# Kernel tuning notes

Hardware: AMD Instinct MI355X
Metric: run time of the kernel (lower is better)

The kernel has to match this reference:

```python
import jax, jax.numpy as jnp
import numpy as np

N_TILE = 50000
N_POI = 50000
E = 200000
IN_F = 128
HID = 256
OUT = 256
HEADS = 8
NEG_SLOPE = 0.2


def gatv2(hs, hd, src, dst, Wsrc, bsrc, Wdst, bdst, attn, n_dst):
    """DGL GATv2Conv: per-edge LeakyReLU(fs_u + fd_v) attention, edge-softmax over
    incoming edges of each dst node, attention-weighted sum of source features.
    Returns (n_dst, H*D) (already flattened, matching .flatten(1))."""
    H, D = attn.shape
    fs = (hs @ Wsrc + bsrc).reshape(-1, H, D)  # (Ns, H, D)
    fd = (hd @ Wdst + bdst).reshape(-1, H, D)  # (Nd, H, D)
    e = jax.nn.leaky_relu(fs[src] + fd[dst], NEG_SLOPE)       # (E, H, D)
    logits = jnp.einsum('ehd,hd->eh', e, attn)                # (E, H)
    # segment softmax over destination neighborhoods
    mx = jax.ops.segment_max(logits, dst, num_segments=n_dst)  # (Nd, H)
    ex = jnp.exp(logits - mx[dst])
    den = jax.ops.segment_sum(ex, dst, num_segments=n_dst)
    alpha = ex / den[dst]                                      # (E, H)
    out = jax.ops.segment_sum(fs[src] * alpha[:, :, None], dst, num_segments=n_dst)
    return out.reshape(n_dst, H * D)


def hetero_layer(ht, hp, Wsrc, bsrc, Wdst, bdst, attn, idx, mean_agg):
    src_road, dst_road, src_tb, dst_tb, src_ct, dst_ct = idx
    m_road = gatv2(ht, ht, src_road, dst_road, Wsrc[0], bsrc[0], Wdst[0], bdst[0], attn[0], N_TILE)
    m_tb = gatv2(hp, ht, src_tb, dst_tb, Wsrc[1], bsrc[1], Wdst[1], bdst[1], attn[1], N_TILE)
    m_ct = gatv2(ht, hp, src_ct, dst_ct, Wsrc[2], bsrc[2], Wdst[2], bdst[2], attn[2], N_POI)
    tile = (m_road + m_tb) * (0.5 if mean_agg else 1.0)  # cross-relation sum/mean
    poi = m_ct  # single relation: sum == mean
    return jax.nn.relu(tile), jax.nn.relu(poi)


def _params(key, fan_in, fan_out, heads, dhead):
    ks = jax.random.split(key, 5)
    s = 1.0 / np.sqrt(fan_in)
    return (jax.random.normal(ks[0], (3, fan_in, fan_out), jnp.float32) * s,
            jnp.zeros((3, fan_out), jnp.float32),
            jax.random.normal(ks[1], (3, fan_in, fan_out), jnp.float32) * s,
            jnp.zeros((3, fan_out), jnp.float32),
            jax.random.normal(ks[2], (3, heads, dhead), jnp.float32) * s)


def setup_inputs() -> dict:
    key = jax.random.key(0)
    ks = jax.random.split(key, 12)
    inp = {
        'x_tile': jax.random.normal(ks[0], (N_TILE, IN_F), jnp.float32),
        'x_poi': jax.random.normal(ks[1], (N_POI, IN_F), jnp.float32),
        'src_road': jax.random.randint(ks[2], (E,), 0, N_TILE, jnp.int32),
        'dst_road': jax.random.randint(ks[3], (E,), 0, N_TILE, jnp.int32),
        'src_tb': jax.random.randint(ks[4], (E,), 0, N_POI, jnp.int32),
        'dst_tb': jax.random.randint(ks[5], (E,), 0, N_TILE, jnp.int32),
        'src_ct': jax.random.randint(ks[6], (E,), 0, N_TILE, jnp.int32),
        'dst_ct': jax.random.randint(ks[7], (E,), 0, N_POI, jnp.int32),
    }
    D = HID // HEADS
    for i, (fi, fo) in enumerate([(IN_F, HID), (HID, HID), (HID, OUT)]):
        Ws, bs, Wd, bd, at = _params(ks[8 + i], fi, fo, HEADS, fo // HEADS)
        inp[f'W_src_{i}'] = Ws; inp[f'b_src_{i}'] = bs
        inp[f'W_dst_{i}'] = Wd; inp[f'b_dst_{i}'] = bd
        inp[f'attn_{i}'] = at
    return inp


def reference(x_tile, x_poi, src_road, dst_road, src_tb, dst_tb, src_ct, dst_ct,
              W_src_0, b_src_0, W_dst_0, b_dst_0, attn_0,
              W_src_1, b_src_1, W_dst_1, b_dst_1, attn_1,
              W_src_2, b_src_2, W_dst_2, b_dst_2, attn_2):
    idx = (src_road, dst_road, src_tb, dst_tb, src_ct, dst_ct)
    ht, hp = hetero_layer(x_tile, x_poi, W_src_0, b_src_0, W_dst_0, b_dst_0, attn_0, idx, mean_agg=False)
    ht, hp = hetero_layer(ht, hp, W_src_1, b_src_1, W_dst_1, b_dst_1, attn_1, idx, mean_agg=True)
    ht, hp = hetero_layer(ht, hp, W_src_2, b_src_2, W_dst_2, b_dst_2, attn_2, idx, mean_agg=False)
    return ht, hp
```

## Files before the change

### kernel.cpp

```cpp
#include <hip/hip_runtime.h>
#include <hip/hip_bf16.h>

typedef __hip_bfloat16 bf16;

#define NT 50000
#define NP 50000
#define NE 200000
#define HH 8
#define DD 32
#define CC 256
#define NBLK 196

#define BM 128
#define BK 32

typedef short s8v __attribute__((ext_vector_type(8)));
typedef float f4v __attribute__((ext_vector_type(4)));

__device__ __forceinline__ float bu2f(unsigned short u) {
  return __uint_as_float(((unsigned)u) << 16);
}
__device__ __forceinline__ unsigned short f2bu(float x) {
  bf16 b = __float2bfloat16(x);
  return *(unsigned short*)&b;
}

__device__ __forceinline__ void gload_lds16(const void* g, void* l) {
  __builtin_amdgcn_global_load_lds(
      (const __attribute__((address_space(1))) void*)g,
      (__attribute__((address_space(3))) void*)l, 16, 0, 0);
}

__global__ __launch_bounds__(256) void cvt_f2b(const float* __restrict__ in,
                                               bf16* __restrict__ out, int n) {
  int i = blockIdx.x * 256 + threadIdx.x;
  if (i < n) out[i] = __float2bfloat16(in[i]);
}

struct WtArgs {
  const float* Ws[3]; const float* Wd[3];
  bf16* W1[3]; bf16* W2[3];
};
__global__ __launch_bounds__(256) void wt_cvt_all(WtArgs a) {
  int l = blockIdx.z, y = blockIdx.y;
  int K = (l == 0) ? 128 : 256;
  int idx = blockIdx.x * 256 + threadIdx.x;
  if (idx >= 256 * K) return;
  int n = idx / K, k = idx - n * K;
  const float* W; bf16* D; int dn;
  if (y == 0)      { W = a.Ws[l];                       D = a.W1[l]; dn = n; }
  else if (y == 1) { W = a.Wd[l];                       D = a.W1[l]; dn = n + 256; }
  else if (y == 2) { W = a.Wd[l] + (size_t)1 * K * 256; D = a.W1[l]; dn = n + 512; }
  else if (y == 3) { W = a.Ws[l] + (size_t)2 * K * 256; D = a.W1[l]; dn = n + 768; }
  else if (y == 4) { W = a.Ws[l] + (size_t)1 * K * 256; D = a.W2[l]; dn = n; }
  else             { W = a.Wd[l] + (size_t)2 * K * 256; D = a.W2[l]; dn = n + 256; }
  D[(size_t)dn * K + k] = __float2bfloat16(W[(size_t)k * 256 + n]);
}

struct BiArgs {
  const float* bs[3]; const float* bd[3];
  float* b1; float* b2;
};
__global__ __launch_bounds__(256) void bias_cat(BiArgs a) {
  int l = blockIdx.y, y = blockIdx.x;
  int n = threadIdx.x;
  float v;
  if (y == 0)      v = a.bs[l][n];
  else if (y == 1) v = a.bd[l][n];
  else if (y == 2) v = a.bd[l][256 + n];
  else if (y == 3) v = a.bs[l][512 + n];
  else if (y == 4) v = a.bs[l][256 + n];
  else             v = a.bd[l][512 + n];
  if (y < 4) a.b1[l * 1024 + y * 256 + n] = v;
  else       a.b2[l * 512 + (y - 4) * 256 + n] = v;
}

__global__ __launch_bounds__(256) void zero_i(int* __restrict__ p, int n) {
  int i = blockIdx.x * 256 + threadIdx.x;
  if (i < n) p[i] = 0;
}

__global__ __launch_bounds__(256) void hist3(
    const int* __restrict__ d0, const int* __restrict__ d1,
    const int* __restrict__ d2, int* __restrict__ deg) {
  int r = blockIdx.y;
  int e = blockIdx.x * 256 + threadIdx.x;
  if (e >= NE) return;
  const int* d = (r == 0) ? d0 : (r == 1) ? d1 : d2;
  atomicAdd(&deg[r * NT + d[e]], 1);
}

__global__ __launch_bounds__(256) void scan_s1(const int* __restrict__ deg,
                                               int* __restrict__ bsum) {
  __shared__ int buf[256];
  int r = blockIdx.y, b = blockIdx.x, t = threadIdx.x;
  int idx = b * 256 + t;
  buf[t] = (idx < NT) ? deg[r * NT + idx] : 0;
  __syncthreads();
  for (int s = 128; s > 0; s >>= 1) {
    if (t < s) buf[t] += buf[t + s];
    __syncthreads();
  }
  if (t == 0) bsum[r * NBLK + b] = buf[0];
}

__global__ __launch_bounds__(256) void scan_s2(
    const int* __restrict__ bsum, int* __restrict__ boff,
    int* __restrict__ offs) {
  __shared__ int buf[256];
  int t = threadIdx.x;
  for (int r = 0; r < 3; r++) {
    int v = (t < NBLK) ? bsum[r * NBLK + t] : 0;
    buf[t] = v;
    __syncthreads();
    for (int s = 1; s < 256; s <<= 1) {
      int u = (t >= s) ? buf[t - s] : 0;
      __syncthreads();
      buf[t] += u;
      __syncthreads();
    }
    if (t < NBLK) boff[r * NBLK + t] = buf[t] - v;
    if (t == 255) offs[(size_t)r * (NT + 1) + NT] = buf[255];
    __syncthreads();
  }
}

__global__ __launch_bounds__(256) void scan_s3(
    const int* __restrict__ deg, const int* __restrict__ boff,
    int* __restrict__ offs, int* __restrict__ cursor) {
  __shared__ int buf[256];
  int r = blockIdx.y, b = blockIdx.x, t = threadIdx.x;
  int idx = b * 256 + t;
  int v = (idx < NT) ? deg[r * NT + idx] : 0;
  buf[t] = v;
  __syncthreads();
  for (int s = 1; s < 256; s <<= 1) {
    int u = (t >= s) ? buf[t - s] : 0;
    __syncthreads();
    buf[t] += u;
    __syncthreads();
  }
  int o = boff[r * NBLK + b] + buf[t] - v;
  if (idx < NT) {
    offs[(size_t)r * (NT + 1) + idx] = o;
    cursor[r * NT + idx] = o;
  }
}

__global__ __launch_bounds__(256) void fill3(
    const int* __restrict__ d0, const int* __restrict__ d1,
    const int* __restrict__ d2, const int* __restrict__ s0,
    const int* __restrict__ s1, const int* __restrict__ s2,
    int* __restrict__ cursor, int* __restrict__ csrc) {
  int r = blockIdx.y;
  int e = blockIdx.x * 256 + threadIdx.x;
  if (e >= NE) return;
  const int* d = (r == 0) ? d0 : (r == 1) ? d1 : d2;
  const int* s = (r == 0) ? s0 : (r == 1) ? s1 : s2;
  int p = atomicAdd(&cursor[r * NT + d[e]], 1);
  csrc[(size_t)r * NE + p] = s[e];
}

__global__ __launch_bounds__(256) void gemm_dual(
    const bf16* __restrict__ A1, const bf16* __restrict__ B1t,
    const float* __restrict__ bias1, bf16* __restrict__ C1, int Nc1,
    const bf16* __restrict__ A2, const bf16* __restrict__ B2t,
    const float* __restrict__ bias2, bf16* __restrict__ C2, int Nc2,
    int M, int K, int NW1, int q8, int r8) {
  __shared__ short LDS[16384];
  int bid = blockIdx.x;
  int xcd = bid & 7, pos = bid >> 3;
  int wg = (xcd < r8 ? xcd * (q8 + 1) : r8 * (q8 + 1) + (xcd - r8) * q8) + pos;

  const bf16* A; const bf16* Bt; const float* bias; bf16* Cout; int Ncols;
  if (wg < NW1) { A = A1; Bt = B1t; bias = bias1; Cout = C1; Ncols = Nc1; }
  else { wg -= NW1; A = A2; Bt = B2t; bias = bias2; Cout = C2; Ncols = Nc2; }
  int nbn = Ncols >> 7;
  int bm = wg / nbn, bn = wg - bm * nbn;

  int t = threadIdx.x;
  int lane = t & 63;
  int wid = t >> 6;
  int wm = wid >> 1, wn = wid & 1;
  int row0 = bm * BM, col0 = bn * BM;

  f4v acc[4][4] = {};

  const bf16* Abase = A + (size_t)row0 * K;
  const bf16* Bbase = Bt + (size_t)col0 * K;
  int wbase = (t & ~63);

  auto stage = [&](int buf, int ks) {
    int kofs = ks * BK;
    #pragma unroll
    for (int j = 0; j < 2; j++) {
      int slot = j * 256 + t;
      int r = slot >> 2;
      int c = (slot & 3) ^ ((slot >> 3) & 3);
      gload_lds16(Abase + (size_t)r * K + kofs + c * 8,
                  &LDS[buf * 4096 + (j * 256 + wbase) * 8]);
    }
    #pragma unroll
    for (int j = 0; j < 2; j++) {
      int slot = j * 256 + t;
      int r = slot >> 2;
      int c = (slot & 3) ^ ((slot >> 3) & 3);
      gload_lds16(Bbase + (size_t)r * K + kofs + c * 8,
                  &LDS[8192 + buf * 4096 + (j * 256 + wbase) * 8]);
    }
  };

  int nk = K / BK;
  int cur = 0;
  stage(0, 0);
  __syncthreads();

  for (int ks = 0; ks < nk; ks++) {
    if (ks + 1 < nk) stage(cur ^ 1, ks + 1);
    int c = lane >> 4;
    int rr = lane & 15;
    s8v af[4], bfv[4];
    #pragma unroll
    for (int mi = 0; mi < 4; mi++) {
      int R = wm * 64 + mi * 16 + rr;
      af[mi] = *(const s8v*)&LDS[cur * 4096 + (R * 4 + (c ^ ((R >> 1) & 3))) * 8];
    }
    #pragma unroll
    for (int ni = 0; ni < 4; ni++) {
      int R = wn * 64 + ni * 16 + rr;
      bfv[ni] = *(const s8v*)&LDS[8192 + cur * 4096 + (R * 4 + (c ^ ((R >> 1) & 3))) * 8];
    }
    #pragma unroll
    for (int mi = 0; mi < 4; mi++)
      #pragma unroll
      for (int ni = 0; ni < 4; ni++)
        acc[mi][ni] = __builtin_amdgcn_mfma_f32_16x16x32_bf16(
            af[mi], bfv[ni], acc[mi][ni], 0, 0, 0);
    __syncthreads();
    cur ^= 1;
  }

  #pragma unroll
  for (int mi = 0; mi < 4; mi++) {
    #pragma unroll
    for (int ni = 0; ni < 4; ni++) {
      int colL = wn * 64 + ni * 16 + (lane & 15);
      float bv = bias[col0 + colL];
      #pragma unroll
      for (int r = 0; r < 4; r++) {
        int rowL = wm * 64 + mi * 16 + (lane >> 4) * 4 + r;
        int chunk = (colL >> 3) ^ (rowL & 7);
        LDS[rowL * 128 + chunk * 8 + (colL & 7)] = f2bu(acc[mi][ni][r] + bv);
      }
    }
  }
  __syncthreads();
  {
    int rowL = t >> 1, hf = t & 1;
    int grow = row0 + rowL;
    if (grow < M) {
      unsigned short* Cu = (unsigned short*)Cout;
      #pragma unroll
      for (int j = 0; j < 8; j++) {
        int chunkL = hf * 8 + j;
        s8v v = *(const s8v*)&LDS[rowL * 128 + (chunkL ^ (rowL & 7)) * 8];
        *(s8v*)&Cu[(size_t)grow * Ncols + col0 + chunkL * 8] = v;
      }
    }
  }
}

__device__ __forceinline__ float edge_logit(
    ushort4 u, float d0, float d1, float d2, float d3, float4 at,
    float& f0, float& f1, float& f2, float& f3) {
  f0 = bu2f(u.x); f1 = bu2f(u.y); f2 = bu2f(u.z); f3 = bu2f(u.w);
  float t0 = f0 + d0; t0 = t0 > 0.f ? t0 : 0.2f * t0;
  float t1 = f1 + d1; t1 = t1 > 0.f ? t1 : 0.2f * t1;
  float t2 = f2 + d2; t2 = t2 > 0.f ? t2 : 0.2f * t2;
  float t3 = f3 + d3; t3 = t3 > 0.f ? t3 : 0.2f * t3;
  float lg = t0 * at.x + t1 * at.y + t2 * at.z + t3 * at.w;
  lg += __shfl_xor(lg, 1);
  lg += __shfl_xor(lg, 2);
  lg += __shfl_xor(lg, 4);
  return lg;
}

__device__ __forceinline__ float4 gat_pass(
    int e0, int e1, const int* __restrict__ csrc,
    const unsigned short* __restrict__ base, size_t stride,
    float d0, float d1, float d2, float d3, float4 at) {
  float m = -1e30f, den = 0.f;
  float a0 = 0.f, a1 = 0.f, a2 = 0.f, a3 = 0.f;
  int e = e0;
  for (; e + 2 <= e1; e += 2) {
    int s0 = csrc[e], s1 = csrc[e + 1];
    ushort4 u0 = *(const ushort4*)(base + (size_t)s0 * stride);
    ushort4 u1 = *(const ushort4*)(base + (size_t)s1 * stride);
    float f0, f1, f2, f3, g0, g1, g2, g3;
    float lg0 = edge_logit(u0, d0, d1, d2, d3, at, f0, f1, f2, f3);
    float lg1 = edge_logit(u1, d0, d1, d2, d3, at, g0, g1, g2, g3);
    float mn = fmaxf(m, fmaxf(lg0, lg1));
    float c = __expf(m - mn);
    float x0 = __expf(lg0 - mn);
    float x1 = __expf(lg1 - mn);
    den = den * c + x0 + x1;
    a0 = a0 * c + x0 * f0 + x1 * g0;
    a1 = a1 * c + x0 * f1 + x1 * g1;
    a2 = a2 * c + x0 * f2 + x1 * g2;
    a3 = a3 * c + x0 * f3 + x1 * g3;
    m = mn;
  }
  if (e < e1) {
    int s0 = csrc[e];
    ushort4 u0 = *(const ushort4*)(base + (size_t)s0 * stride);
    float f0, f1, f2, f3;
    float lg0 = edge_logit(u0, d0, d1, d2, d3, at, f0, f1, f2, f3);
    float mn = fmaxf(m, lg0);
    float c = __expf(m - mn);
    float x0 = __expf(lg0 - mn);
    den = den * c + x0;
    a0 = a0 * c + x0 * f0;
    a1 = a1 * c + x0 * f1;
    a2 = a2 * c + x0 * f2;
    a3 = a3 * c + x0 * f3;
  }
  float inv = (den > 0.f) ? 1.f / den : 0.f;
  return make_float4(a0 * inv, a1 * inv, a2 * inv, a3 * inv);
}

__global__ __launch_bounds__(256) void node_gat_all(
    const int* __restrict__ offs, const int* __restrict__ csrc,
    const bf16* __restrict__ F1, const bf16* __restrict__ F2,
    const float* __restrict__ attnL, float scale,
    bf16* __restrict__ ht_n, bf16* __restrict__ hp_n,
    float* __restrict__ outT, float* __restrict__ outP) {
  int gw = blockIdx.x * 4 + (threadIdx.x >> 6);
  int lane = threadIdx.x & 63;
  int off = (lane >> 3) * DD + (lane & 7) * 4;
  const unsigned short* F1u = (const unsigned short*)F1;
  const unsigned short* F2u = (const unsigned short*)F2;

  if (gw < NT) {
    ushort4 udA = *(const ushort4*)(F1u + (size_t)gw * 1024 + 256 + off);
    float4 atA = *(const float4*)(attnL + off);
    float4 ra = gat_pass(offs[gw], offs[gw + 1], csrc, F1u + off, 1024,
                         bu2f(udA.x), bu2f(udA.y), bu2f(udA.z), bu2f(udA.w), atA);

    const int* offsB = offs + (NT + 1);
    ushort4 udB = *(const ushort4*)(F1u + (size_t)gw * 1024 + 512 + off);
    float4 atB = *(const float4*)(attnL + 256 + off);
    float4 rb = gat_pass(offsB[gw], offsB[gw + 1], csrc + NE, F2u + off, 512,
                         bu2f(udB.x), bu2f(udB.y), bu2f(udB.z), bu2f(udB.w), atB);

    float v0 = (ra.x + rb.x) * scale; v0 = v0 > 0.f ? v0 : 0.f;
    float v1 = (ra.y + rb.y) * scale; v1 = v1 > 0.f ? v1 : 0.f;
    float v2 = (ra.z + rb.z) * scale; v2 = v2 > 0.f ? v2 : 0.f;
    float v3 = (ra.w + rb.w) * scale; v3 = v3 > 0.f ? v3 : 0.f;

    size_t base = (size_t)gw * CC + off;
    *(ushort4*)((unsigned short*)ht_n + base) =
        make_ushort4(f2bu(v0), f2bu(v1), f2bu(v2), f2bu(v3));
    if (outT) *(float4*)(outT + base) = make_float4(v0, v1, v2, v3);
  } else {
    int w = gw - NT;
    const int* offsC = offs + 2 * (NT + 1);
    ushort4 ud = *(const ushort4*)(F2u + (size_t)w * 512 + 256 + off);
    float4 at = *(const float4*)(attnL + 512 + off);
    float4 r = gat_pass(offsC[w], offsC[w + 1], csrc + 2 * (size_t)NE,
                        F1u + 768 + off, 1024,
                        bu2f(ud.x), bu2f(ud.y), bu2f(ud.z), bu2f(ud.w), at);

    float v0 = r.x > 0.f ? r.x : 0.f;
    float v1 = r.y > 0.f ? r.y : 0.f;
    float v2 = r.z > 0.f ? r.z : 0.f;
    float v3 = r.w > 0.f ? r.w : 0.f;

    size_t base = (size_t)w * CC + off;
    *(ushort4*)((unsigned short*)hp_n + base) =
        make_ushort4(f2bu(v0), f2bu(v1), f2bu(v2), f2bu(v3));
    if (outP) *(float4*)(outP + base) = make_float4(v0, v1, v2, v3);
  }
}

extern "C" void kernel_launch(void* const* d_in, const int* in_sizes, int n_in,
                              void* d_out, int out_size, void* d_ws, size_t ws_size,
                              hipStream_t stream) {
  const float* x_tile = (const float*)d_in[0];
  const float* x_poi  = (const float*)d_in[1];
  const int* src_road = (const int*)d_in[2];
  const int* dst_road = (const int*)d_in[3];
  const int* src_tb   = (const int*)d_in[4];
  const int* dst_tb   = (const int*)d_in[5];
  const int* src_ct   = (const int*)d_in[6];
  const int* dst_ct   = (const int*)d_in[7];
  const float* Wsrc[3] = {(const float*)d_in[8],  (const float*)d_in[13], (const float*)d_in[18]};
  const float* bsrc[3] = {(const float*)d_in[9],  (const float*)d_in[14], (const float*)d_in[19]};
  const float* Wdst[3] = {(const float*)d_in[10], (const float*)d_in[15], (const float*)d_in[20]};
  const float* bdst[3] = {(const float*)d_in[11], (const float*)d_in[16], (const float*)d_in[21]};
  const float* attn[3] = {(const float*)d_in[12], (const float*)d_in[17], (const float*)d_in[22]};

  bf16* hbuf = (bf16*)d_ws;
  bf16* ht2[2] = {hbuf, hbuf + (size_t)NT * CC};
  bf16* hp2[2] = {hbuf + 2 * (size_t)NT * CC, hbuf + 3 * (size_t)NT * CC};
  bf16* F1 = hbuf + 4 * (size_t)NT * CC;
  bf16* F2 = F1 + (size_t)NT * 1024;
  int* offs = (int*)(F2 + (size_t)NT * 512);
  int* deg  = offs + 3 * (NT + 1);
  int* csrc = deg + 3 * NT;
  int* bsum = csrc + (size_t)3 * NE;
  int* boff = bsum + 3 * NBLK;
  uintptr_t wp = ((uintptr_t)(boff + 3 * NBLK) + 63) & ~(uintptr_t)63;
  bf16* W1c[3], *W2c[3];
  {
    bf16* w = (bf16*)wp;
    for (int l = 0; l < 3; l++) {
      int K = (l == 0) ? 128 : 256;
      W1c[l] = w; w += (size_t)1024 * K;
      W2c[l] = w; w += (size_t)512 * K;
    }
    wp = (uintptr_t)w;
  }
  float* b1 = (float*)((wp + 63) & ~(uintptr_t)63);
  float* b2 = b1 + 3 * 1024;

  cvt_f2b<<<(NT * 128 + 255) / 256, 256, 0, stream>>>(x_tile, ht2[0], NT * 128);
  cvt_f2b<<<(NP * 128 + 255) / 256, 256, 0, stream>>>(x_poi, hp2[0], NP * 128);

  {
    WtArgs wa;
    BiArgs ba;
    for (int l = 0; l < 3; l++) {
      wa.Ws[l] = Wsrc[l]; wa.Wd[l] = Wdst[l];
      wa.W1[l] = W1c[l];  wa.W2[l] = W2c[l];
      ba.bs[l] = bsrc[l]; ba.bd[l] = bdst[l];
    }
    ba.b1 = b1; ba.b2 = b2;
    dim3 gw(256, 6, 3);
    wt_cvt_all<<<gw, 256, 0, stream>>>(wa);
    dim3 gb(6, 3);
    bias_cat<<<gb, 256, 0, stream>>>(ba);
  }

  zero_i<<<(3 * NT + 255) / 256, 256, 0, stream>>>(deg, 3 * NT);
  {
    dim3 ge((NE + 255) / 256, 3);
    hist3<<<ge, 256, 0, stream>>>(dst_road, dst_tb, dst_ct, deg);
    dim3 gn(NBLK, 3);
    scan_s1<<<gn, 256, 0, stream>>>(deg, bsum);
    scan_s2<<<1, 256, 0, stream>>>(bsum, boff, offs);
    scan_s3<<<gn, 256, 0, stream>>>(deg, boff, offs, deg);
    fill3<<<ge, 256, 0, stream>>>(dst_road, dst_tb, dst_ct,
                                  src_road, src_tb, src_ct, deg, csrc);
  }

  int nbm = (NT + BM - 1) / BM;
  int cb = 0;
  for (int l = 0; l < 3; l++) {
    int K = (l == 0) ? 128 : 256;
    bf16* ht_c = ht2[cb], *hp_c = hp2[cb];
    bf16* ht_n = ht2[cb ^ 1], *hp_n = hp2[cb ^ 1];
    float st = (l == 1) ? 0.5f : 1.0f;
    float* outT = (l == 2) ? (float*)d_out : nullptr;
    float* outP = (l == 2) ? ((float*)d_out + (size_t)NT * CC) : nullptr;

    int NW1 = 8 * nbm, NW2 = 4 * nbm;
    int NW = NW1 + NW2, q8 = NW / 8, r8 = NW % 8;
    gemm_dual<<<NW, 256, 0, stream>>>(
        ht_c, W1c[l], b1 + l * 1024, F1, 1024,
        hp_c, W2c[l], b2 + l * 512,  F2, 512,
        NT, K, NW1, q8, r8);

    node_gat_all<<<(NT + NP) / 4, 256, 0, stream>>>(
        offs, csrc, F1, F2, attn[l], st, ht_n, hp_n, outT, outP);

    cb ^= 1;
  }
}
```

Measured before the change: 626.7 us.

## Enlarge GEMM tiles to 256x256 with 8 warps and unroll edge loop by four

The dual projection GEMM moves from 128x128 tiles with 256 threads to 256x256 tiles with 512 threads. Each warp now computes 128x64, which raises arithmetic intensity per LDS load and cuts the number of workgroups. The epilogue drops its LDS-staged vector stores and writes scalar bf16 values straight to global memory, so stores are less coalesced. The GAT aggregation loop is unrolled from two to four edges per iteration to put more gathers in flight, and the tail becomes a loop that correctly updates the running max.

Result: slower. 761.8 us (+21.6%).

```diff
diff --git a/kernel.cpp b/kernel.cpp
--- a/kernel.cpp
+++ b/kernel.cpp
@@ -10,9 +10,6 @@
 #define DD 32
 #define CC 256
 #define NBLK 196
-
-#define BM 128
-#define BK 32
 
 typedef short s8v __attribute__((ext_vector_type(8)));
 typedef float f4v __attribute__((ext_vector_type(4)));
@@ -161,110 +158,95 @@
   csrc[(size_t)r * NE + p] = s[e];
 }
 
-__global__ __launch_bounds__(256) void gemm_dual(
+__global__ __launch_bounds__(512, 2) void gemm256(
     const bf16* __restrict__ A1, const bf16* __restrict__ B1t,
-    const float* __restrict__ bias1, bf16* __restrict__ C1, int Nc1,
+    const float* __restrict__ bias1, bf16* __restrict__ C1,
     const bf16* __restrict__ A2, const bf16* __restrict__ B2t,
-    const float* __restrict__ bias2, bf16* __restrict__ C2, int Nc2,
-    int M, int K, int NW1, int q8, int r8) {
-  __shared__ short LDS[16384];
+    const float* __restrict__ bias2, bf16* __restrict__ C2,
+    int M, int K, int q8, int r8) {
+  __shared__ short LDS[2][2][8192];
   int bid = blockIdx.x;
   int xcd = bid & 7, pos = bid >> 3;
   int wg = (xcd < r8 ? xcd * (q8 + 1) : r8 * (q8 + 1) + (xcd - r8) * q8) + pos;
-
-  const bf16* A; const bf16* Bt; const float* bias; bf16* Cout; int Ncols;
-  if (wg < NW1) { A = A1; Bt = B1t; bias = bias1; Cout = C1; Ncols = Nc1; }
-  else { wg -= NW1; A = A2; Bt = B2t; bias = bias2; Cout = C2; Ncols = Nc2; }
-  int nbn = Ncols >> 7;
-  int bm = wg / nbn, bn = wg - bm * nbn;
+  int bm = wg / 6, bn = wg - bm * 6;
+
+  const bf16* A; const bf16* Bt; const float* bias; bf16* Cout; int Ncols, col0;
+  if (bn < 4) { A = A1; Bt = B1t + (size_t)bn * 256 * K; bias = bias1; Cout = C1; Ncols = 1024; col0 = bn * 256; }
+  else { A = A2; Bt = B2t + (size_t)(bn - 4) * 256 * K; bias = bias2; Cout = C2; Ncols = 512; col0 = (bn - 4) * 256; }
 
   int t = threadIdx.x;
   int lane = t & 63;
   int wid = t >> 6;
-  int wm = wid >> 1, wn = wid & 1;
-  int row0 = bm * BM, col0 = bn * BM;
-
-  f4v acc[4][4] = {};
+  int wm = wid >> 2, wn = wid & 3;
+  int row0 = bm * 256;
+  int wbase = t & ~63;
+
+  f4v acc[8][4] = {};
 
   const bf16* Abase = A + (size_t)row0 * K;
-  const bf16* Bbase = Bt + (size_t)col0 * K;
-  int wbase = (t & ~63);
-
-  auto stage = [&](int buf, int ks) {
-    int kofs = ks * BK;
+
+  auto stage = [&](int buf, int kt) {
+    int kofs = kt * 32;
     #pragma unroll
     for (int j = 0; j < 2; j++) {
-      int slot = j * 256 + t;
-      int r = slot >> 2;
-      int c = (slot & 3) ^ ((slot >> 3) & 3);
-      gload_lds16(Abase + (size_t)r * K + kofs + c * 8,
-                  &LDS[buf * 4096 + (j * 256 + wbase) * 8]);
+      int s = j * 512 + t;
+      int row = s >> 2, ch = s & 3;
+      int sch = ch ^ ((row >> 1) & 3);
+      gload_lds16(Abase + (size_t)row * K + kofs + sch * 8,
+                  &LDS[buf][0][(j * 512 + wbase) * 8]);
     }
     #pragma unroll
     for (int j = 0; j < 2; j++) {
-      int slot = j * 256 + t;
-      int r = slot >> 2;
-      int c = (slot & 3) ^ ((slot >> 3) & 3);
-      gload_lds16(Bbase + (size_t)r * K + kofs + c * 8,
-                  &LDS[8192 + buf * 4096 + (j * 256 + wbase) * 8]);
+      int s = j * 512 + t;
+      int row = s >> 2, ch = s & 3;
+      int sch = ch ^ ((row >> 1) & 3);
+      gload_lds16(Bt + (size_t)row * K + kofs + sch * 8,
+                  &LDS[buf][1][(j * 512 + wbase) * 8]);
     }
   };
 
-  int nk = K / BK;
-  int cur = 0;
+  int nk = K / 32;
   stage(0, 0);
   __syncthreads();
 
-  for (int ks = 0; ks < nk; ks++) {
-    if (ks + 1 < nk) stage(cur ^ 1, ks + 1);
-    int c = lane >> 4;
+  int cur = 0;
+  for (int kt = 0; kt < nk; kt++) {
+    if (kt + 1 < nk) stage(cur ^ 1, kt + 1);
+    int ch = lane >> 4;
     int rr = lane & 15;
-    s8v af[4], bfv[4];
-    #pragma unroll
-    for (int mi = 0; mi < 4; mi++) {
-      int R = wm * 64 + mi * 16 + rr;
-      af[mi] = *(const s8v*)&LDS[cur * 4096 + (R * 4 + (c ^ ((R >> 1) & 3))) * 8];
-    }
-    #pragma unroll
-    for (int ni = 0; ni < 4; ni++) {
-      int R = wn * 64 + ni * 16 + rr;
-      bfv[ni] = *(const s8v*)&LDS[8192 + cur * 4096 + (R * 4 + (c ^ ((R >> 1) & 3))) * 8];
-    }
-    #pragma unroll
-    for (int mi = 0; mi < 4; mi++)
+    s8v af[8], bfv[4];
+    #pragma unroll
+    for (int mf = 0; mf < 8; mf++) {
+      int row = wm * 128 + mf * 16 + rr;
+      af[mf] = *(const s8v*)&LDS[cur][0][(row * 4 + (ch ^ ((row >> 1) & 3))) * 8];
+    }
+    #pragma unroll
+    for (int nf = 0; nf < 4; nf++) {
+      int row = wn * 64 + nf * 16 + rr;
+      bfv[nf] = *(const s8v*)&LDS[cur][1][(row * 4 + (ch ^ ((row >> 1) & 3))) * 8];
+    }
+    #pragma unroll
+    for (int mf = 0; mf < 8; mf++)
       #pragma unroll
-      for (int ni = 0; ni < 4; ni++)
-        acc[mi][ni] = __builtin_amdgcn_mfma_f32_16x16x32_bf16(
-            af[mi], bfv[ni], acc[mi][ni], 0, 0, 0);
+      for (int nf = 0; nf < 4; nf++)
+        acc[mf][nf] = __builtin_amdgcn_mfma_f32_16x16x32_bf16(
+            af[mf], bfv[nf], acc[mf][nf], 0, 0, 0);
     __syncthreads();
     cur ^= 1;
   }
 
+  unsigned short* Cu = (unsigned short*)Cout;
   #pragma unroll
-  for (int mi = 0; mi < 4; mi++) {
-    #pragma unroll
-    for (int ni = 0; ni < 4; ni++) {
-      int colL = wn * 64 + ni * 16 + (lane & 15);
-      float bv = bias[col0 + colL];
+  for (int nf = 0; nf < 4; nf++) {
+    int col = col0 + wn * 64 + nf * 16 + (lane & 15);
+    float bv = bias[col];
+    #pragma unroll
+    for (int mf = 0; mf < 8; mf++) {
+      int row = row0 + wm * 128 + mf * 16 + (lane >> 4) * 4;
       #pragma unroll
       for (int r = 0; r < 4; r++) {
-        int rowL = wm * 64 + mi * 16 + (lane >> 4) * 4 + r;
-        int chunk = (colL >> 3) ^ (rowL & 7);
-        LDS[rowL * 128 + chunk * 8 + (colL & 7)] = f2bu(acc[mi][ni][r] + bv);
-      }
-    }
-  }
-  __syncthreads();
-  {
-    int rowL = t >> 1, hf = t & 1;
-    int grow = row0 + rowL;
-    if (grow < M) {
-      unsigned short* Cu = (unsigned short*)Cout;
-      #pragma unroll
-      for (int j = 0; j < 8; j++) {
-        int chunkL = hf * 8 + j;
-        s8v v = *(const s8v*)&LDS[rowL * 128 + (chunkL ^ (rowL & 7)) * 8];
-        *(s8v*)&Cu[(size_t)grow * Ncols + col0 + chunkL * 8] = v;
+        if (row + r < M)
+          Cu[(size_t)(row + r) * Ncols + col] = f2bu(acc[mf][nf][r] + bv);
       }
     }
   }
@@ -292,25 +274,31 @@
   float m = -1e30f, den = 0.f;
   float a0 = 0.f, a1 = 0.f, a2 = 0.f, a3 = 0.f;
   int e = e0;
-  for (; e + 2 <= e1; e += 2) {
-    int s0 = csrc[e], s1 = csrc[e + 1];
+  for (; e + 4 <= e1; e += 4) {
+    int s0 = csrc[e], s1 = csrc[e + 1], s2 = csrc[e + 2], s3 = csrc[e + 3];
     ushort4 u0 = *(const ushort4*)(base + (size_t)s0 * stride);
     ushort4 u1 = *(const ushort4*)(base + (size_t)s1 * stride);
-    float f0, f1, f2, f3, g0, g1, g2, g3;
+    ushort4 u2 = *(const ushort4*)(base + (size_t)s2 * stride);
+    ushort4 u3 = *(const ushort4*)(base + (size_t)s3 * stride);
+    float f0, f1, f2, f3, g0, g1, g2, g3, h0, h1, h2, h3, i0, i1, i2, i3;
     float lg0 = edge_logit(u0, d0, d1, d2, d3, at, f0, f1, f2, f3);
     float lg1 = edge_logit(u1, d0, d1, d2, d3, at, g0, g1, g2, g3);
-    float mn = fmaxf(m, fmaxf(lg0, lg1));
+    float lg2 = edge_logit(u2, d0, d1, d2, d3, at, h0, h1, h2, h3);
+    float lg3 = edge_logit(u3, d0, d1, d2, d3, at, i0, i1, i2, i3);
+    float mn = fmaxf(fmaxf(fmaxf(lg0, lg1), fmaxf(lg2, lg3)), m);
     float c = __expf(m - mn);
     float x0 = __expf(lg0 - mn);
     float x1 = __expf(lg1 - mn);
-    den = den * c + x0 + x1;
-    a0 = a0 * c + x0 * f0 + x1 * g0;
-    a1 = a1 * c + x0 * f1 + x1 * g1;
-    a2 = a2 * c + x0 * f2 + x1 * g2;
-    a3 = a3 * c + x0 * f3 + x1 * g3;
+    float x2 = __expf(lg2 - mn);
+    float x3 = __expf(lg3 - mn);
+    den = den * c + x0 + x1 + x2 + x3;
+    a0 = a0 * c + x0 * f0 + x1 * g0 + x2 * h0 + x3 * i0;
+    a1 = a1 * c + x0 * f1 + x1 * g1 + x2 * h1 + x3 * i1;
+    a2 = a2 * c + x0 * f2 + x1 * g2 + x2 * h2 + x3 * i2;
+    a3 = a3 * c + x0 * f3 + x1 * g3 + x2 * h3 + x3 * i3;
     m = mn;
   }
-  if (e < e1) {
+  for (; e < e1; ++e) {
     int s0 = csrc[e];
     ushort4 u0 = *(const ushort4*)(base + (size_t)s0 * stride);
     float f0, f1, f2, f3;
@@ -323,6 +311,7 @@
     a1 = a1 * c + x0 * f1;
     a2 = a2 * c + x0 * f2;
     a3 = a3 * c + x0 * f3;
+    m = mn;
   }
   float inv = (den > 0.f) ? 1.f / den : 0.f;
   return make_float4(a0 * inv, a1 * inv, a2 * inv, a3 * inv);
@@ -453,7 +442,6 @@
                                   src_road, src_tb, src_ct, deg, csrc);
   }
 
-  int nbm = (NT + BM - 1) / BM;
   int cb = 0;
   for (int l = 0; l < 3; l++) {
     int K = (l == 0) ? 128 : 256;
@@ -463,12 +451,11 @@
     float* outT = (l == 2) ? (float*)d_out : nullptr;
     float* outP = (l == 2) ? ((float*)d_out + (size_t)NT * CC) : nullptr;
 
-    int NW1 = 8 * nbm, NW2 = 4 * nbm;
-    int NW = NW1 + NW2, q8 = NW / 8, r8 = NW % 8;
-    gemm_dual<<<NW, 256, 0, stream>>>(
-        ht_c, W1c[l], b1 + l * 1024, F1, 1024,
-        hp_c, W2c[l], b2 + l * 512,  F2, 512,
-        NT, K, NW1, q8, r8);
+    int NW = NBLK * 6, q8 = NW / 8, r8 = NW % 8;
+    gemm256<<<NW, 512, 0, stream>>>(
+        ht_c, W1c[l], b1 + l * 1024, F1,
+        hp_c, W2c[l], b2 + l * 512,  F2,
+        NT, K, q8, r8);
 
     node_gat_all<<<(NT + NP) / 4, 256, 0, stream>>>(
         offs, csrc, F1, F2, attn[l], st, ht_n, hp_n, outT, outP);
```
